# Kernel tuning notes

Measured on AMD Instinct MI355X. Metric: run time of the kernel, lower is better.

## Reference

```python
import jax, jax.numpy as jnp
import numpy as np

B, S, D, A = 16, 2048, 512, 512

def setup_inputs() -> dict:
    key = jax.random.key(0)
    ks = jax.random.split(key, 7)
    scale = 1.0 / np.sqrt(D)
    return {
        "query": jax.random.normal(ks[0], (B, S, D), dtype=jnp.float32),
        "key_": jax.random.normal(ks[1], (B, S, D), dtype=jnp.float32),
        "value": jax.random.normal(ks[2], (B, S, D), dtype=jnp.float32),
        "Wq": jax.random.normal(ks[3], (D, A), dtype=jnp.float32) * scale,
        "Wk": jax.random.normal(ks[4], (D, A), dtype=jnp.float32) * scale,
        "Wv": jax.random.normal(ks[5], (D, A), dtype=jnp.float32) * scale,
        "Ws": jax.random.normal(ks[6], (A, 1), dtype=jnp.float32) * (1.0 / np.sqrt(A)),
    }

def reference(query, key_, value, Wq, Wk, Wv, Ws):
    # Dense projections (no bias): [B,S,D] @ [D,A] -> [B,S,A]
    q = jnp.einsum("bsd,da->bsa", query, Wq)
    k = jnp.einsum("bsd,da->bsa", key_, Wk)
    v = jnp.einsum("bsd,da->bsa", value, Wv)
    # Additive (Bahdanau) scores: tanh(q+k) @ Ws -> [B,S]
    scores = jnp.einsum("bsa,a->bs", jnp.tanh(q + k), Ws[:, 0])
    attention_weights = jax.nn.softmax(scores, axis=1)[..., None]  # [B,S,1]
    context_vector = jnp.sum(attention_weights * v, axis=1)        # [B,A]
    return context_vector, attention_weights
```

## Files before the change

### kernel.cpp

```cpp
#include <hip/hip_runtime.h>
#include <hip/hip_bf16.h>
#include <stdint.h>

#define B_ 16
#define S_ 2048
#define D_ 512
#define A_ 512

typedef __attribute__((ext_vector_type(4))) float f32x4;
typedef __attribute__((ext_vector_type(8))) short bf16x8;

__device__ inline unsigned short f2bf(float f) {
  union { float f; unsigned int u; } c; c.f = f;
  unsigned int u = c.u;
  unsigned int r = (u + 0x7fffu + ((u >> 16) & 1u)) >> 16;
  return (unsigned short)r;
}

__device__ inline unsigned pk2bf(float x, float y) {
  __hip_bfloat162 p = __float22bfloat162_rn(float2{x, y});
  union { __hip_bfloat162 h; unsigned u; } c; c.h = p;
  return c.u;
}

__device__ inline float fast_tanh(float x) {
  float e = __expf(2.0f * x);
  return 1.0f - 2.0f * __builtin_amdgcn_rcpf(e + 1.0f);
}

__device__ inline void gload_lds16(const void* g, void* l) {
  __builtin_amdgcn_global_load_lds((const __attribute__((address_space(1))) void*)g,
                                   (__attribute__((address_space(3))) void*)l, 16, 0, 0);
}

__global__ __launch_bounds__(256) void k0_pack_w(const float* __restrict__ Wq,
                                                 const float* __restrict__ Wk,
                                                 unsigned short* __restrict__ WT) {
  __shared__ unsigned short tile[64][65];
  int bid = blockIdx.x;
  int dt = bid & 15, at = bid >> 4;
  int d0 = dt * 64, a0 = at * 64;
  int t = threadIdx.x;
  int col = t & 63, rbase = t >> 6;
#pragma unroll
  for (int r8 = 0; r8 < 16; ++r8) {
    int row = r8 * 4 + rbase;
    int dcat = d0 + row;
    float f = (dcat < 512) ? Wq[(size_t)dcat * 512 + a0 + col]
                           : Wk[(size_t)(dcat - 512) * 512 + a0 + col];
    tile[row][col] = f2bf(f);
  }
  __syncthreads();
#pragma unroll
  for (int r8 = 0; r8 < 16; ++r8) {
    int arow = r8 * 4 + rbase;
    WT[(size_t)(a0 + arow) * 1024 + d0 + col] = tile[col][arow];
  }
}

__global__ __launch_bounds__(512, 2) void k1_scores(
    const float* __restrict__ Q, const float* __restrict__ K,
    const unsigned short* __restrict__ WT, const float* __restrict__ Wsv,
    float* __restrict__ score) {
  __shared__ unsigned short Al[2][128 * 32];
  __shared__ unsigned short Bl[2][512 * 32];

  const int t = threadIdx.x;
  const int lane = t & 63, w = t >> 6;
  const int frow = lane & 15, fsl = lane >> 4;
  const int row0 = (int)blockIdx.x * 128;

  const int ar = t >> 2, ak = (t & 3) * 8;
  const int abyte = ar * 64 + (((t & 3) ^ ((ar >> 1) & 3)) * 16);

  float4 rA0[2], rA1[2];

  auto issueA = [&](int p, float4* r) {
    const float* src = (p < 16) ? Q : K;
    const float* ap = src + (size_t)(row0 + ar) * 512 + ((p * 32) & 511) + ak;
    r[0] = *(const float4*)(ap);
    r[1] = *(const float4*)(ap + 4);
  };
  auto writeA = [&](const float4* r, int buf) {
    uint4 d;
    d.x = pk2bf(r[0].x, r[0].y);
    d.y = pk2bf(r[0].z, r[0].w);
    d.z = pk2bf(r[1].x, r[1].y);
    d.w = pk2bf(r[1].z, r[1].w);
    *(uint4*)((char*)&Al[buf][0] + abyte) = d;
  };
  auto stageB = [&](int p, int buf) {
#pragma unroll
    for (int q = 0; q < 4; ++q) {
      int pc = (w * 4 + q) * 64 + lane;
      int row = pc >> 2;
      int sl = (pc & 3) ^ ((row >> 1) & 3);
      const char* g = (const char*)WT + (size_t)row * 2048 + p * 64 + sl * 16;
      gload_lds16(g, (char*)&Bl[buf][0] + (size_t)(w * 4 + q) * 1024);
    }
  };

  f32x4 acc[8][4];
#pragma unroll
  for (int m = 0; m < 8; ++m)
#pragma unroll
    for (int n = 0; n < 4; ++n) acc[m][n] = (f32x4){0.f, 0.f, 0.f, 0.f};

  const int ch = (fsl ^ ((frow >> 1) & 3)) * 16;

  auto doMfma = [&](int CUR) {
    bf16x8 af[8], bfr[4];
#pragma unroll
    for (int m = 0; m < 8; ++m)
      af[m] = *(const bf16x8*)((const char*)&Al[CUR][0] + (m * 16 + frow) * 64 + ch);
#pragma unroll
    for (int n = 0; n < 4; ++n)
      bfr[n] = *(const bf16x8*)((const char*)&Bl[CUR][0] + (w * 64 + n * 16 + frow) * 64 + ch);
    __builtin_amdgcn_s_setprio(1);
#pragma unroll
    for (int m = 0; m < 8; ++m)
#pragma unroll
      for (int n = 0; n < 4; ++n)
        acc[m][n] = __builtin_amdgcn_mfma_f32_16x16x32_bf16(af[m], bfr[n], acc[m][n], 0, 0, 0);
    __builtin_amdgcn_s_setprio(0);
  };

  issueA(0, rA0);
  stageB(0, 0);
  writeA(rA0, 0);
  issueA(1, rA1);
  __syncthreads();

  auto phase = [&](int p, int CUR, float4* rCur, const float4* rNext) {
    stageB(p + 1, CUR ^ 1);
    issueA(p + 2, rCur);
    doMfma(CUR);
    writeA(rNext, CUR ^ 1);
    __syncthreads();
  };

  for (int kt2 = 0; kt2 < 15; ++kt2) {
    phase(2 * kt2 + 0, 0, rA0, rA1);
    phase(2 * kt2 + 1, 1, rA1, rA0);
  }

  stageB(31, 1);
  doMfma(0);
  writeA(rA1, 1);
  __syncthreads();
  doMfma(1);

  float wsv[4];
#pragma unroll
  for (int n = 0; n < 4; ++n) wsv[n] = Wsv[w * 64 + n * 16 + frow];
  __syncthreads();
  float* scw = (float*)&Al[0][0];
#pragma unroll
  for (int m = 0; m < 8; ++m) {
#pragma unroll
    for (int ii = 0; ii < 4; ++ii) {
      float s = 0.f;
#pragma unroll
      for (int n = 0; n < 4; ++n)
        s += fast_tanh(acc[m][n][ii]) * wsv[n];
      s += __shfl_xor(s, 1);
      s += __shfl_xor(s, 2);
      s += __shfl_xor(s, 4);
      s += __shfl_xor(s, 8);
      if (frow == 0) scw[w * 128 + m * 16 + fsl * 4 + ii] = s;
    }
  }
  __syncthreads();
  if (t < 128) {
    float s = 0.f;
#pragma unroll
    for (int ww = 0; ww < 8; ++ww) s += scw[ww * 128 + t];
    score[row0 + t] = s;
  }
}

__global__ __launch_bounds__(256) void k3_vsum(const float* __restrict__ value,
                                               const float* __restrict__ score,
                                               float* __restrict__ upart,
                                               float* __restrict__ outw) {
  int bid = blockIdx.x;
  int dh = bid & 1, sc = (bid >> 1) & 15, b = bid >> 5;
  int t = threadIdx.x;
  int lane = t & 63, wave = t >> 6;
  int dg = t & 63, sg = t >> 6;
  __shared__ float red[4], red2[4];
  __shared__ float wl[128];
  __shared__ f32x4 redv[4][64];

  float v[8];
  float mx = -1e30f;
#pragma unroll
  for (int e = 0; e < 8; ++e) {
    float p = score[(size_t)b * S_ + e * 256 + t];
    v[e] = p;
    mx = fmaxf(mx, p);
  }
  for (int off = 1; off < 64; off <<= 1) mx = fmaxf(mx, __shfl_xor(mx, off));
  if (lane == 0) red[wave] = mx;
  __syncthreads();
  mx = fmaxf(fmaxf(red[0], red[1]), fmaxf(red[2], red[3]));
  float sum = 0.f;
#pragma unroll
  for (int e = 0; e < 8; ++e) sum += expf(v[e] - mx);
  for (int off = 1; off < 64; off <<= 1) sum += __shfl_xor(sum, off);
  if (lane == 0) red2[wave] = sum;
  __syncthreads();
  sum = red2[0] + red2[1] + red2[2] + red2[3];
  float inv = 1.f / sum;

  int s0 = sc * 128;
  if (t < 128) {
    size_t o = (size_t)b * S_ + s0 + t;
    float ww = expf(score[o] - mx) * inv;
    wl[t] = ww;
    if (dh == 0) outw[o] = ww;
  }
  __syncthreads();

  const float* vp = value + ((size_t)b * S_ + s0) * 512 + dh * 256 + dg * 4;
  f32x4 a = (f32x4){0.f, 0.f, 0.f, 0.f};
  for (int s = sg; s < 128; s += 4) {
    float4 v4 = *(const float4*)(vp + (size_t)s * 512);
    float ws = wl[s];
    a[0] += ws * v4.x; a[1] += ws * v4.y; a[2] += ws * v4.z; a[3] += ws * v4.w;
  }
  redv[sg][dg] = a;
  __syncthreads();
  if (sg == 0) {
    f32x4 r = redv[0][dg] + redv[1][dg] + redv[2][dg] + redv[3][dg];
    float* dst = upart + (size_t)(sc * 16 + b) * 512 + dh * 256 + dg * 4;
    dst[0] = r[0]; dst[1] = r[1]; dst[2] = r[2]; dst[3] = r[3];
  }
}

__global__ __launch_bounds__(256) void k4_ctx(const float* __restrict__ upart,
                                              const float* __restrict__ Wv,
                                              float* __restrict__ out) {
  int b = blockIdx.x >> 2, q = blockIdx.x & 3;
  int t = threadIdx.x;
  int col = q * 128 + (t & 127), dhf = t >> 7;
  __shared__ float ul[512];
  __shared__ float part[2][128];
  for (int i = t; i < 512; i += 256) {
    float u = 0.f;
#pragma unroll
    for (int c = 0; c < 16; ++c) u += upart[(size_t)(c * 16 + b) * 512 + i];
    ul[i] = u;
  }
  __syncthreads();
  float acc = 0.f;
#pragma unroll 8
  for (int d = dhf * 256; d < dhf * 256 + 256; ++d)
    acc += ul[d] * Wv[(size_t)d * 512 + col];
  part[dhf][t & 127] = acc;
  __syncthreads();
  if (dhf == 0)
    out[(size_t)b * 512 + col] = part[0][t & 127] + part[1][t & 127];
}

extern "C" void kernel_launch(void* const* d_in, const int* in_sizes, int n_in,
                              void* d_out, int out_size, void* d_ws, size_t ws_size,
                              hipStream_t stream) {
  const float* Q  = (const float*)d_in[0];
  const float* Kk = (const float*)d_in[1];
  const float* V  = (const float*)d_in[2];
  const float* Wq = (const float*)d_in[3];
  const float* Wk = (const float*)d_in[4];
  const float* Wv = (const float*)d_in[5];
  const float* Ws = (const float*)d_in[6];
  float* out = (float*)d_out;

  char* ws = (char*)d_ws;
  unsigned short* WT = (unsigned short*)ws;
  float* score = (float*)(ws + (1 << 20));
  float* upart = (float*)(ws + (1 << 20) + (512 << 10));

  float* outw = out + B_ * A_;

  k0_pack_w<<<dim3(128), dim3(256), 0, stream>>>(Wq, Wk, WT);
  k1_scores<<<dim3(256), dim3(512), 0, stream>>>(Q, Kk, WT, Ws, score);
  k3_vsum<<<dim3(512), dim3(256), 0, stream>>>(V, score, upart, outw);
  k4_ctx<<<dim3(64), dim3(256), 0, stream>>>(upart, Wv, out);
}
```

Measured before the change: 88.01 us.

## Retile score GEMM to 256x256 blocks with split-column partial scores

The fused projection-and-score kernel now computes 256-row by 256-column output tiles with K-steps of 64 instead of 128 rows by all 512 columns. Because tanh is applied per column and then reduced with Ws, each column half produces a partial score that is written separately. The softmax kernel sums the two partials. This cuts per-block weight staging and halves the number of K iterations and barriers, and a block-index swizzle tries to keep the two column blocks that share a row strip close in L2. In exchange, each row strip of Q and K is read twice from global memory, LDS use grows to 128KB so only one block fits per CU, and waits now drain all loads before each barrier.

Result: slower. 121.4 us (+37.9%).

```diff
diff --git a/kernel.cpp b/kernel.cpp
--- a/kernel.cpp
+++ b/kernel.cpp
@@ -6,6 +6,7 @@
 #define S_ 2048
 #define D_ 512
 #define A_ 512
+#define M_TOT (B_ * S_)
 
 typedef __attribute__((ext_vector_type(4))) float f32x4;
 typedef __attribute__((ext_vector_type(8))) short bf16x8;
@@ -58,44 +59,53 @@
   }
 }
 
-__global__ __launch_bounds__(512, 2) void k1_scores(
+__global__ __launch_bounds__(512, 1) void k1_scores(
     const float* __restrict__ Q, const float* __restrict__ K,
     const unsigned short* __restrict__ WT, const float* __restrict__ Wsv,
-    float* __restrict__ score) {
-  __shared__ unsigned short Al[2][128 * 32];
-  __shared__ unsigned short Bl[2][512 * 32];
+    float* __restrict__ partial) {
+  __shared__ unsigned short Al[2][256 * 64];
+  __shared__ unsigned short Bl[2][256 * 64];
 
   const int t = threadIdx.x;
   const int lane = t & 63, w = t >> 6;
   const int frow = lane & 15, fsl = lane >> 4;
-  const int row0 = (int)blockIdx.x * 128;
-
-  const int ar = t >> 2, ak = (t & 3) * 8;
-  const int abyte = ar * 64 + (((t & 3) ^ ((ar >> 1) & 3)) * 16);
-
-  float4 rA0[2], rA1[2];
-
-  auto issueA = [&](int p, float4* r) {
-    const float* src = (p < 16) ? Q : K;
-    const float* ap = src + (size_t)(row0 + ar) * 512 + ((p * 32) & 511) + ak;
-    r[0] = *(const float4*)(ap);
-    r[1] = *(const float4*)(ap + 4);
+  const int wr = w >> 2, wc = w & 3;
+
+  const int bid = (int)blockIdx.x;
+  const int wg = (bid & 7) * 32 + (bid >> 3);
+  const int strip = wg >> 1, cb = wg & 1;
+  const int row0 = strip * 256, col0 = cb * 256;
+
+  const int ar = t >> 1, hc = t & 1;
+
+  float4 rA[8];
+
+  auto issueA = [&](int kt) {
+    const float* src = (kt < 8) ? Q : K;
+    const float* ap = src + (size_t)(row0 + ar) * 512 + (kt & 7) * 64 + hc * 32;
+#pragma unroll
+    for (int i = 0; i < 8; ++i) rA[i] = *(const float4*)(ap + i * 4);
   };
-  auto writeA = [&](const float4* r, int buf) {
-    uint4 d;
-    d.x = pk2bf(r[0].x, r[0].y);
-    d.y = pk2bf(r[0].z, r[0].w);
-    d.z = pk2bf(r[1].x, r[1].y);
-    d.w = pk2bf(r[1].z, r[1].w);
-    *(uint4*)((char*)&Al[buf][0] + abyte) = d;
+  auto writeA = [&](int buf) {
+    char* base = (char*)&Al[buf][0] + ar * 128;
+#pragma unroll
+    for (int i = 0; i < 4; ++i) {
+      uint4 d;
+      d.x = pk2bf(rA[2 * i].x, rA[2 * i].y);
+      d.y = pk2bf(rA[2 * i].z, rA[2 * i].w);
+      d.z = pk2bf(rA[2 * i + 1].x, rA[2 * i + 1].y);
+      d.w = pk2bf(rA[2 * i + 1].z, rA[2 * i + 1].w);
+      int chunk = hc * 4 + i;
+      *(uint4*)(base + ((chunk ^ (ar & 7)) * 16)) = d;
+    }
   };
-  auto stageB = [&](int p, int buf) {
+  auto stageB = [&](int kt, int buf) {
 #pragma unroll
     for (int q = 0; q < 4; ++q) {
-      int pc = (w * 4 + q) * 64 + lane;
-      int row = pc >> 2;
-      int sl = (pc & 3) ^ ((row >> 1) & 3);
-      const char* g = (const char*)WT + (size_t)row * 2048 + p * 64 + sl * 16;
+      int p = (w * 4 + q) * 64 + lane;
+      int row = p >> 3, c = p & 7;
+      const char* g = (const char*)WT + (size_t)(col0 + row) * 2048
+                      + kt * 128 + ((c ^ (row & 7)) * 16);
       gload_lds16(g, (char*)&Bl[buf][0] + (size_t)(w * 4 + q) * 1024);
     }
   };
@@ -106,53 +116,55 @@
 #pragma unroll
     for (int n = 0; n < 4; ++n) acc[m][n] = (f32x4){0.f, 0.f, 0.f, 0.f};
 
-  const int ch = (fsl ^ ((frow >> 1) & 3)) * 16;
-
   auto doMfma = [&](int CUR) {
-    bf16x8 af[8], bfr[4];
-#pragma unroll
-    for (int m = 0; m < 8; ++m)
-      af[m] = *(const bf16x8*)((const char*)&Al[CUR][0] + (m * 16 + frow) * 64 + ch);
-#pragma unroll
-    for (int n = 0; n < 4; ++n)
-      bfr[n] = *(const bf16x8*)((const char*)&Bl[CUR][0] + (w * 64 + n * 16 + frow) * 64 + ch);
+    bf16x8 af[2][8], bfr[2][4];
+#pragma unroll
+    for (int ks = 0; ks < 2; ++ks) {
+#pragma unroll
+      for (int m = 0; m < 8; ++m) {
+        int r = wr * 128 + m * 16 + frow;
+        af[ks][m] = *(const bf16x8*)((const char*)&Al[CUR][0] + r * 128
+                      + (((ks * 4 + fsl) ^ (r & 7)) * 16));
+      }
+#pragma unroll
+      for (int n = 0; n < 4; ++n) {
+        int r = wc * 64 + n * 16 + frow;
+        bfr[ks][n] = *(const bf16x8*)((const char*)&Bl[CUR][0] + r * 128
+                       + (((ks * 4 + fsl) ^ (r & 7)) * 16));
+      }
+    }
     __builtin_amdgcn_s_setprio(1);
 #pragma unroll
-    for (int m = 0; m < 8; ++m)
-#pragma unroll
-      for (int n = 0; n < 4; ++n)
-        acc[m][n] = __builtin_amdgcn_mfma_f32_16x16x32_bf16(af[m], bfr[n], acc[m][n], 0, 0, 0);
+    for (int ks = 0; ks < 2; ++ks)
+#pragma unroll
+      for (int m = 0; m < 8; ++m)
+#pragma unroll
+        for (int n = 0; n < 4; ++n)
+          acc[m][n] = __builtin_amdgcn_mfma_f32_16x16x32_bf16(
+              af[ks][m], bfr[ks][n], acc[m][n], 0, 0, 0);
     __builtin_amdgcn_s_setprio(0);
   };
 
-  issueA(0, rA0);
+  issueA(0);
   stageB(0, 0);
-  writeA(rA0, 0);
-  issueA(1, rA1);
-  __syncthreads();
-
-  auto phase = [&](int p, int CUR, float4* rCur, const float4* rNext) {
-    stageB(p + 1, CUR ^ 1);
-    issueA(p + 2, rCur);
-    doMfma(CUR);
-    writeA(rNext, CUR ^ 1);
-    __syncthreads();
-  };
-
-  for (int kt2 = 0; kt2 < 15; ++kt2) {
-    phase(2 * kt2 + 0, 0, rA0, rA1);
-    phase(2 * kt2 + 1, 1, rA1, rA0);
-  }
-
-  stageB(31, 1);
-  doMfma(0);
-  writeA(rA1, 1);
-  __syncthreads();
+  writeA(0);
+  asm volatile("s_waitcnt vmcnt(0) lgkmcnt(0)" ::: "memory");
+  __builtin_amdgcn_s_barrier();
+
+  for (int kt = 0; kt < 15; ++kt) {
+    const int cur = kt & 1;
+    issueA(kt + 1);
+    stageB(kt + 1, cur ^ 1);
+    doMfma(cur);
+    writeA(cur ^ 1);
+    asm volatile("s_waitcnt vmcnt(0) lgkmcnt(0)" ::: "memory");
+    __builtin_amdgcn_s_barrier();
+  }
   doMfma(1);
 
   float wsv[4];
 #pragma unroll
-  for (int n = 0; n < 4; ++n) wsv[n] = Wsv[w * 64 + n * 16 + frow];
+  for (int n = 0; n < 4; ++n) wsv[n] = Wsv[col0 + wc * 64 + n * 16 + frow];
   __syncthreads();
   float* scw = (float*)&Al[0][0];
 #pragma unroll
@@ -167,20 +179,19 @@
       s += __shfl_xor(s, 2);
       s += __shfl_xor(s, 4);
       s += __shfl_xor(s, 8);
-      if (frow == 0) scw[w * 128 + m * 16 + fsl * 4 + ii] = s;
+      if (frow == 0)
+        scw[wc * 256 + wr * 128 + m * 16 + fsl * 4 + ii] = s;
     }
   }
   __syncthreads();
-  if (t < 128) {
-    float s = 0.f;
-#pragma unroll
-    for (int ww = 0; ww < 8; ++ww) s += scw[ww * 128 + t];
-    score[row0 + t] = s;
+  if (t < 256) {
+    float s = scw[t] + scw[256 + t] + scw[512 + t] + scw[768 + t];
+    partial[(size_t)cb * M_TOT + row0 + t] = s;
   }
 }
 
 __global__ __launch_bounds__(256) void k3_vsum(const float* __restrict__ value,
-                                               const float* __restrict__ score,
+                                               const float* __restrict__ partial,
                                                float* __restrict__ upart,
                                                float* __restrict__ outw) {
   int bid = blockIdx.x;
@@ -196,7 +207,8 @@
   float mx = -1e30f;
 #pragma unroll
   for (int e = 0; e < 8; ++e) {
-    float p = score[(size_t)b * S_ + e * 256 + t];
+    size_t o = (size_t)b * S_ + e * 256 + t;
+    float p = partial[o] + partial[M_TOT + o];
     v[e] = p;
     mx = fmaxf(mx, p);
   }
@@ -216,7 +228,7 @@
   int s0 = sc * 128;
   if (t < 128) {
     size_t o = (size_t)b * S_ + s0 + t;
-    float ww = expf(score[o] - mx) * inv;
+    float ww = expf(partial[o] + partial[M_TOT + o] - mx) * inv;
     wl[t] = ww;
     if (dh == 0) outw[o] = ww;
   }
@@ -277,13 +289,13 @@
 
   char* ws = (char*)d_ws;
   unsigned short* WT = (unsigned short*)ws;
-  float* score = (float*)(ws + (1 << 20));
-  float* upart = (float*)(ws + (1 << 20) + (512 << 10));
+  float* partial = (float*)(ws + (1 << 20));
+  float* upart   = (float*)(ws + (1 << 20) + (512 << 10));
 
   float* outw = out + B_ * A_;
 
   k0_pack_w<<<dim3(128), dim3(256), 0, stream>>>(Wq, Wk, WT);
-  k1_scores<<<dim3(256), dim3(512), 0, stream>>>(Q, Kk, WT, Ws, score);
-  k3_vsum<<<dim3(512), dim3(256), 0, stream>>>(V, score, upart, outw);
+  k1_scores<<<dim3(256), dim3(512), 0, stream>>>(Q, Kk, WT, Ws, partial);
+  k3_vsum<<<dim3(512), dim3(256), 0, stream>>>(V, partial, upart, outw);
   k4_ctx<<<dim3(64), dim3(256), 0, stream>>>(upart, Wv, out);
 }
```

## Load weight fragments directly from global into registers, drop LDS staging of B

Applied to the files above, without the earlier changes.

The B operand (packed Wq/Wk weights) is no longer staged through LDS with global_load_lds. Each wave now loads its MFMA B fragments straight from global memory, relying on cache hits because all blocks share the same weights. The full __syncthreads calls are replaced by explicit s_waitcnt plus s_barrier so that the prefetched A loads can stay in flight across the barrier. This cuts LDS use and could improve occupancy, but B loads now sit on the MFMA critical path with global latency and no double buffering.

New measurement: 100.0 us. 13.7% more time.

```diff
diff --git a/kernel.cpp b/kernel.cpp
--- a/kernel.cpp
+++ b/kernel.cpp
@@ -26,11 +26,6 @@
 __device__ inline float fast_tanh(float x) {
   float e = __expf(2.0f * x);
   return 1.0f - 2.0f * __builtin_amdgcn_rcpf(e + 1.0f);
-}
-
-__device__ inline void gload_lds16(const void* g, void* l) {
-  __builtin_amdgcn_global_load_lds((const __attribute__((address_space(1))) void*)g,
-                                   (__attribute__((address_space(3))) void*)l, 16, 0, 0);
 }
 
 __global__ __launch_bounds__(256) void k0_pack_w(const float* __restrict__ Wq,
@@ -63,7 +58,7 @@
     const unsigned short* __restrict__ WT, const float* __restrict__ Wsv,
     float* __restrict__ score) {
   __shared__ unsigned short Al[2][128 * 32];
-  __shared__ unsigned short Bl[2][512 * 32];
+  __shared__ float scw[8][128];
 
   const int t = threadIdx.x;
   const int lane = t & 63, w = t >> 6;
@@ -89,16 +84,8 @@
     d.w = pk2bf(r[1].z, r[1].w);
     *(uint4*)((char*)&Al[buf][0] + abyte) = d;
   };
-  auto stageB = [&](int p, int buf) {
-#pragma unroll
-    for (int q = 0; q < 4; ++q) {
-      int pc = (w * 4 + q) * 64 + lane;
-      int row = pc >> 2;
-      int sl = (pc & 3) ^ ((row >> 1) & 3);
-      const char* g = (const char*)WT + (size_t)row * 2048 + p * 64 + sl * 16;
-      gload_lds16(g, (char*)&Bl[buf][0] + (size_t)(w * 4 + q) * 1024);
-    }
-  };
+
+  const char* bbase = (const char*)WT + (size_t)(w * 64 + frow) * 2048 + fsl * 16;
 
   f32x4 acc[8][4];
 #pragma unroll
@@ -108,14 +95,15 @@
 
   const int ch = (fsl ^ ((frow >> 1) & 3)) * 16;
 
-  auto doMfma = [&](int CUR) {
-    bf16x8 af[8], bfr[4];
+  auto doMfma = [&](int p, int CUR) {
+    bf16x8 bfr[4];
+#pragma unroll
+    for (int n = 0; n < 4; ++n)
+      bfr[n] = *(const bf16x8*)(bbase + (size_t)n * 16 * 2048 + p * 64);
+    bf16x8 af[8];
 #pragma unroll
     for (int m = 0; m < 8; ++m)
       af[m] = *(const bf16x8*)((const char*)&Al[CUR][0] + (m * 16 + frow) * 64 + ch);
-#pragma unroll
-    for (int n = 0; n < 4; ++n)
-      bfr[n] = *(const bf16x8*)((const char*)&Bl[CUR][0] + (w * 64 + n * 16 + frow) * 64 + ch);
     __builtin_amdgcn_s_setprio(1);
 #pragma unroll
     for (int m = 0; m < 8; ++m)
@@ -126,17 +114,18 @@
   };
 
   issueA(0, rA0);
-  stageB(0, 0);
+  __builtin_amdgcn_sched_barrier(0);
+  issueA(1, rA1);
   writeA(rA0, 0);
-  issueA(1, rA1);
-  __syncthreads();
+  asm volatile("s_waitcnt vmcnt(2) lgkmcnt(0)" ::: "memory");
+  __builtin_amdgcn_s_barrier();
 
   auto phase = [&](int p, int CUR, float4* rCur, const float4* rNext) {
-    stageB(p + 1, CUR ^ 1);
     issueA(p + 2, rCur);
-    doMfma(CUR);
+    doMfma(p, CUR);
     writeA(rNext, CUR ^ 1);
-    __syncthreads();
+    asm volatile("s_waitcnt vmcnt(2) lgkmcnt(0)" ::: "memory");
+    __builtin_amdgcn_s_barrier();
   };
 
   for (int kt2 = 0; kt2 < 15; ++kt2) {
@@ -144,17 +133,15 @@
     phase(2 * kt2 + 1, 1, rA1, rA0);
   }
 
-  stageB(31, 1);
-  doMfma(0);
+  doMfma(30, 0);
   writeA(rA1, 1);
-  __syncthreads();
-  doMfma(1);
+  asm volatile("s_waitcnt vmcnt(0) lgkmcnt(0)" ::: "memory");
+  __builtin_amdgcn_s_barrier();
+  doMfma(31, 1);
 
   float wsv[4];
 #pragma unroll
   for (int n = 0; n < 4; ++n) wsv[n] = Wsv[w * 64 + n * 16 + frow];
-  __syncthreads();
-  float* scw = (float*)&Al[0][0];
 #pragma unroll
   for (int m = 0; m < 8; ++m) {
 #pragma unroll
@@ -167,14 +154,14 @@
       s += __shfl_xor(s, 2);
       s += __shfl_xor(s, 4);
       s += __shfl_xor(s, 8);
-      if (frow == 0) scw[w * 128 + m * 16 + fsl * 4 + ii] = s;
+      if (frow == 0) scw[w][m * 16 + fsl * 4 + ii] = s;
     }
   }
   __syncthreads();
   if (t < 128) {
     float s = 0.f;
 #pragma unroll
-    for (int ww = 0; ww < 8; ++ww) s += scw[ww * 128 + t];
+    for (int ww = 0; ww < 8; ++ww) s += scw[ww][t];
     score[row0 + t] = s;
   }
 }
```
